# Optimization experiments

Hardware: AMD Instinct MI355X
Metric: run time of the kernel (lower is better)

Reference implementation:

```python
import jax, jax.numpy as jnp
import numpy as np

D_MODEL = 1024
D_INNER = 2048      # expand=2
D_STATE = 128
NHEADS = 32
HEADDIM = 64
DCONV = 4
CONV_DIM = D_INNER + 2 * D_STATE                 # x, B, C channels through conv
D_IN_PROJ = 2 * D_INNER + 2 * D_STATE + NHEADS   # z, xBC, dt
NBLOCKS = 4


def _mlp(x, w1, b1, w2, b2):
    # MLP(2, in, out): Linear(in,in) -> ReLU -> Linear(in,out)
    return jax.nn.relu(x @ w1 + b1) @ w2 + b2


def _mamba2_block(u, Wi, cw, cb, dtb, Alog, Dsk, nw, Wo):
    B, L, _ = u.shape
    zxbcdt = u @ Wi                                        # [B,L,D_IN_PROJ]
    z, xBC, dt = jnp.split(zxbcdt, [D_INNER, D_INNER + CONV_DIM], axis=-1)
    # causal depthwise conv1d, kernel 4
    pad = jnp.pad(xBC, ((0, 0), (DCONV - 1, 0), (0, 0)))
    conv = cb
    for k in range(DCONV):
        conv = conv + pad[:, k:k + L, :] * cw[:, k]
    xBC = jax.nn.silu(conv)
    xh, Bm, Cm = jnp.split(xBC, [D_INNER, D_INNER + D_STATE], axis=-1)
    dt = jax.nn.softplus(dt + dtb)                         # [B,L,H]
    A = -jnp.exp(Alog)                                     # [H], negative
    xh = xh.reshape(B, L, NHEADS, HEADDIM)

    def step(h, inp):
        x_t, dt_t, b_t, c_t = inp                          # [B,H,P],[B,H],[B,N],[B,N]
        dA = jnp.exp(dt_t * A)                             # [B,H]
        h = h * dA[..., None, None] + (dt_t[..., None] * x_t)[..., None] * b_t[:, None, None, :]
        y = jnp.einsum('bhpn,bn->bhp', h, c_t)
        return h, y

    h0 = jnp.zeros((B, NHEADS, HEADDIM, D_STATE), u.dtype)
    _, ys = jax.lax.scan(step, h0, (xh.transpose(1, 0, 2, 3), dt.transpose(1, 0, 2),
                                    Bm.transpose(1, 0, 2), Cm.transpose(1, 0, 2)))
    y = ys.transpose(1, 0, 2, 3) + Dsk[None, None, :, None] * xh   # D skip per head
    y = y.reshape(B, L, D_INNER)
    y = y * jax.nn.silu(z)                                 # gated RMSNorm (gate before norm)
    y = y * jax.lax.rsqrt(jnp.mean(y * y, axis=-1, keepdims=True) + 1e-5) * nw
    return y @ Wo


def setup_inputs() -> dict:
    key = jax.random.key(0)
    ks = jax.random.split(key, 16)
    B, S, STATE = 4, 512, 510
    s = 0.02
    return {
        'x': jax.random.normal(ks[0], (B, S, STATE), jnp.float32),
        'steps_left': jax.random.uniform(ks[1], (B, S, 1), jnp.float32) * 100.0,
        'current_r': jax.random.normal(ks[2], (B, S, 1), jnp.float32),
        'mlp_in_w1': jax.random.normal(ks[3], (STATE + 2, STATE + 2), jnp.float32) * s,
        'mlp_in_b1': jnp.zeros((STATE + 2,), jnp.float32),
        'mlp_in_w2': jax.random.normal(ks[4], (STATE + 2, D_MODEL), jnp.float32) * s,
        'mlp_in_b2': jnp.zeros((D_MODEL,), jnp.float32),
        'W_in': jax.random.normal(ks[5], (NBLOCKS, D_MODEL, D_IN_PROJ), jnp.float32) * s,
        'conv_w': jax.random.normal(ks[6], (NBLOCKS, CONV_DIM, DCONV), jnp.float32) * 0.2,
        'conv_b': jnp.zeros((NBLOCKS, CONV_DIM), jnp.float32),
        'dt_bias': jax.random.normal(ks[7], (NBLOCKS, NHEADS), jnp.float32) * 0.1,
        'A_log': jnp.log(jax.random.uniform(ks[8], (NBLOCKS, NHEADS), jnp.float32, 1.0, 16.0)),
        'D_skip': jnp.ones((NBLOCKS, NHEADS), jnp.float32),
        'norm_w': jnp.ones((NBLOCKS, D_INNER), jnp.float32),
        'W_out': jax.random.normal(ks[9], (NBLOCKS, D_INNER, D_MODEL), jnp.float32) * s,
        'mlp_out_w1': jax.random.normal(ks[10], (D_MODEL, D_MODEL), jnp.float32) * s,
        'mlp_out_b1': jnp.zeros((D_MODEL,), jnp.float32),
        'mlp_out_w2': jax.random.normal(ks[11], (D_MODEL, 1), jnp.float32) * s,
        'mlp_out_b2': jnp.zeros((1,), jnp.float32),
    }


def reference(x, steps_left, current_r,
              mlp_in_w1, mlp_in_b1, mlp_in_w2, mlp_in_b2,
              W_in, conv_w, conv_b, dt_bias, A_log, D_skip, norm_w, W_out,
              mlp_out_w1, mlp_out_b1, mlp_out_w2, mlp_out_b2):
    h = jnp.concatenate([x, steps_left, current_r], axis=-1)   # [B,S,state+2]
    h = _mlp(h, mlp_in_w1, mlp_in_b1, mlp_in_w2, mlp_in_b2)
    for i in range(NBLOCKS):
        h = _mamba2_block(h, W_in[i], conv_w[i], conv_b[i], dt_bias[i],
                          A_log[i], D_skip[i], norm_w[i], W_out[i])
    return _mlp(h, mlp_out_w1, mlp_out_b1, mlp_out_w2, mlp_out_b2)  # [B,S,1]
```

## Files before the change

### kernel.cpp

```cpp
#include <hip/hip_runtime.h>
#include <hip/hip_bf16.h>
#include <math.h>

#define D_MODEL   1024
#define D_INNER   2048
#define D_STATE   128
#define NHEADS    32
#define HEADDIM   64
#define DCONV     4
#define CONV_DIM  (D_INNER + 2 * D_STATE)
#define D_IN_PROJ (2 * D_INNER + 2 * D_STATE + NHEADS)
#define NBLOCKS   4
#define BATCH     4
#define SEQ       512
#define NTOK      (BATCH * SEQ)
#define STATE_IN  510
#define NPAD_IN   4480
#define NSEG      8
#define SEGLEN    64
#define NBH       (BATCH * NHEADS)
#define OFF_B     D_INNER
#define OFF_C     (D_INNER + D_STATE)
#define OFF_DT    (D_IN_PROJ - NHEADS)

typedef _Float16 half8_t __attribute__((ext_vector_type(8)));
typedef float f32x4_t  __attribute__((ext_vector_type(4)));
typedef unsigned short us;
typedef unsigned short us8 __attribute__((ext_vector_type(8)));

__device__ __forceinline__ us f2h(float f) {
    _Float16 h = (_Float16)f;
    return __builtin_bit_cast(us, h);
}
__device__ __forceinline__ float h2f(us u) {
    return (float)__builtin_bit_cast(_Float16, u);
}
__device__ __forceinline__ void gl2lds16(const us* gp, us* lp) {
    __builtin_amdgcn_global_load_lds(
        (const __attribute__((address_space(1))) unsigned int*)(gp),
        (__attribute__((address_space(3))) unsigned int*)(lp), 16, 0, 0);
}

__global__ void concat_kernel(const float* __restrict__ x,
                              const float* __restrict__ steps,
                              const float* __restrict__ curr,
                              us* __restrict__ hcat)
{
    int idx = blockIdx.x * 256 + threadIdx.x;
    if (idx >= NTOK * 512) return;
    int bl = idx >> 9;
    int c  = idx & 511;
    float v;
    if (c < STATE_IN)       v = x[(size_t)bl * STATE_IN + c];
    else if (c == STATE_IN) v = steps[bl];
    else                    v = curr[bl];
    hcat[idx] = f2h(v);
}

#define NT_TRANS 6976
__global__ __launch_bounds__(256)
void transpose_all_kernel(const float* __restrict__ mi_w1, const float* __restrict__ mi_w2,
                          const float* __restrict__ W_in, const float* __restrict__ W_out,
                          const float* __restrict__ mo_w1,
                          us* __restrict__ wt_mi1, us* __restrict__ wt_mi2,
                          us* __restrict__ wt_in, us* __restrict__ wt_out,
                          us* __restrict__ wt_mo1)
{
    int bid = blockIdx.x;
    const float* W; us* WT; int K, N, ntx, r;
    if (bid < 64)        { W = mi_w1; WT = wt_mi1; K = 512;  N = 512;  ntx = 8;  r = bid; }
    else if (bid < 192)  { W = mi_w2; WT = wt_mi2; K = 512;  N = 1024; ntx = 16; r = bid - 64; }
    else if (bid < 4672) {
        int rel = bid - 192, i = rel / 1120;
        r = rel - i * 1120;
        W  = W_in  + (size_t)i * D_MODEL * D_IN_PROJ;
        WT = wt_in + (size_t)i * NPAD_IN * 1024;
        K = 1024; N = D_IN_PROJ; ntx = 70;
    }
    else if (bid < 6720) {
        int rel = bid - 4672, i = rel / 512;
        r = rel - i * 512;
        W  = W_out  + (size_t)i * D_INNER * D_MODEL;
        WT = wt_out + (size_t)i * 1024 * 2048;
        K = 2048; N = 1024; ntx = 16;
    }
    else { W = mo_w1; WT = wt_mo1; K = 1024; N = 1024; ntx = 16; r = bid - 6720; }
    int n0 = (r % ntx) * 64, k0 = (r / ntx) * 64;

    __shared__ float tile[64][65];
    int t = threadIdx.x;
    int kl = t >> 4;
    int nl = (t & 15) * 4;
#pragma unroll
    for (int it = 0; it < 4; ++it) {
        int k = kl + it * 16;
        float4 v = make_float4(0.f, 0.f, 0.f, 0.f);
        if (n0 + nl < N) v = *(const float4*)(W + (size_t)(k0 + k) * N + n0 + nl);
        tile[k][nl + 0] = v.x; tile[k][nl + 1] = v.y;
        tile[k][nl + 2] = v.z; tile[k][nl + 3] = v.w;
    }
    __syncthreads();
    int a  = t & 7;
    int nr = t >> 3;
#pragma unroll
    for (int s = 0; s < 2; ++s) {
        int n = nr + s * 32;
        us8 o;
#pragma unroll
        for (int j = 0; j < 8; ++j) o[j] = f2h(tile[a * 8 + j][n]);
        *(us8*)(WT + (size_t)(n0 + n) * K + k0 + a * 8) = o;
    }
}

#define PHASE(TT, CUR, STG)                                                     \
    {                                                                           \
        if ((TT) == NT - 1)                                                     \
            asm volatile("s_waitcnt vmcnt(0)" ::: "memory");                    \
        else if constexpr (BM / 64 + BN / 64 == 4)                              \
            asm volatile("s_waitcnt vmcnt(4)" ::: "memory");                    \
        else if constexpr (BM / 64 + BN / 64 == 3)                              \
            asm volatile("s_waitcnt vmcnt(3)" ::: "memory");                    \
        else                                                                    \
            asm volatile("s_waitcnt vmcnt(2)" ::: "memory");                    \
        __builtin_amdgcn_s_barrier();                                           \
        if ((TT) + 2 < NT) stage(STG, ((TT) + 2) << 5);                         \
        half8_t af[TI], bfr[4];                                                 \
        _Pragma("unroll")                                                       \
        for (int ti = 0; ti < TI; ++ti) {                                       \
            int rr = wr + ti * 16 + l16;                                        \
            af[ti] = *(const half8_t*)&Al[CUR][rr * 32 + ((g ^ ((rr >> 2) & 3)) * 8)]; \
        }                                                                       \
        _Pragma("unroll")                                                       \
        for (int tj = 0; tj < 4; ++tj) {                                        \
            int rr = wc + tj * 16 + l16;                                        \
            bfr[tj] = *(const half8_t*)&Bl[CUR][rr * 32 + ((g ^ ((rr >> 2) & 3)) * 8)]; \
        }                                                                       \
        _Pragma("unroll")                                                       \
        for (int ti = 0; ti < TI; ++ti)                                         \
            _Pragma("unroll")                                                   \
            for (int tj = 0; tj < 4; ++tj)                                      \
                acc[ti][tj] = __builtin_amdgcn_mfma_f32_16x16x32_f16(           \
                    af[ti], bfr[tj], acc[ti][tj], 0, 0, 0);                     \
    }

template<int BM, int BN, int TI>
__global__ __launch_bounds__(256)
void mfma_gemm_f16(const us* __restrict__ A, const us* __restrict__ BT,
                   const float* __restrict__ bias, us* __restrict__ C,
                   int N, int K, int relu)
{
    __shared__ __attribute__((aligned(16))) us Al[3][BM * 32];
    __shared__ __attribute__((aligned(16))) us Bl[3][BN * 32];
    const int tid = threadIdx.x, lane = tid & 63, wave = tid >> 6;
    const int g = lane >> 4, l16 = lane & 15;
    const int wr = (BN == 128) ? (wave >> 1) * 64 : wave * (BM / 4);
    const int wc = (BN == 128) ? (wave & 1) * 64 : 0;
    const int m0 = blockIdx.y * BM, n0 = blockIdx.x * BN;
    const int lrow = lane >> 2;
    const int lcol = ((lane & 3) ^ ((lrow >> 2) & 3)) * 8;

    f32x4_t acc[TI][4];
    const f32x4_t zero = {0.f, 0.f, 0.f, 0.f};
#pragma unroll
    for (int i = 0; i < TI; ++i)
#pragma unroll
        for (int j = 0; j < 4; ++j) acc[i][j] = zero;

    const us* abase = A  + (size_t)m0 * K;
    const us* bbase = BT + (size_t)n0 * K;

    auto stage = [&](int buf, int k0) {
#pragma unroll
        for (int s = 0; s < BM / 64; ++s) {
            int rb = wave * (BM / 4) + s * 16;
            gl2lds16(abase + (size_t)(rb + lrow) * K + k0 + lcol, &Al[buf][rb * 32]);
        }
#pragma unroll
        for (int s = 0; s < BN / 64; ++s) {
            int rb = wave * (BN / 4) + s * 16;
            gl2lds16(bbase + (size_t)(rb + lrow) * K + k0 + lcol, &Bl[buf][rb * 32]);
        }
    };

    const int NT = K >> 5;
    stage(0, 0);
    stage(1, 32);

    for (int t = 0; t < NT; t += 3) {
        PHASE(t, 0, 2)
        if (t + 1 < NT) PHASE(t + 1, 1, 0)
        if (t + 2 < NT) PHASE(t + 2, 2, 1)
    }

#pragma unroll
    for (int tj = 0; tj < 4; ++tj) {
        int col = n0 + wc + tj * 16 + l16;
        if (col >= N) continue;
        float bv = bias ? bias[col] : 0.f;
#pragma unroll
        for (int ti = 0; ti < TI; ++ti) {
            int rbase = m0 + wr + ti * 16 + g * 4;
#pragma unroll
            for (int r = 0; r < 4; ++r) {
                float v = acc[ti][tj][r] + bv;
                if (relu) v = fmaxf(v, 0.f);
                C[(size_t)(rbase + r) * N + col] = f2h(v);
            }
        }
    }
}

__global__ __launch_bounds__(256)
void conv_silu_kernel(const us* __restrict__ zxbcdt,
                      const float* __restrict__ cw,
                      const float* __restrict__ cb,
                      us* __restrict__ xBCc)
{
    int idx = blockIdx.x * 256 + threadIdx.x;
    if (idx >= NTOK * (CONV_DIM / 4)) return;
    int cq = idx % (CONV_DIM / 4);
    int bl = idx / (CONV_DIM / 4);
    int b  = bl >> 9;
    int l  = bl & 511;
    int c  = cq * 4;
    float4 w0 = *(const float4*)&cw[(c + 0) * DCONV];
    float4 w1 = *(const float4*)&cw[(c + 1) * DCONV];
    float4 w2 = *(const float4*)&cw[(c + 2) * DCONV];
    float4 w3 = *(const float4*)&cw[(c + 3) * DCONV];
    float4 bb = *(const float4*)&cb[c];
    float a0 = bb.x, a1 = bb.y, a2 = bb.z, a3 = bb.w;
    const us* base = zxbcdt + (size_t)(b * SEQ) * D_IN_PROJ + D_INNER + c;
#pragma unroll
    for (int k = 0; k < DCONV; ++k) {
        int ll = l + k - (DCONV - 1);
        if (ll >= 0) {
            ushort4 u = *(const ushort4*)(base + (size_t)ll * D_IN_PROJ);
            a0 = fmaf(h2f(u.x), ((const float*)&w0)[k], a0);
            a1 = fmaf(h2f(u.y), ((const float*)&w1)[k], a1);
            a2 = fmaf(h2f(u.z), ((const float*)&w2)[k], a2);
            a3 = fmaf(h2f(u.w), ((const float*)&w3)[k], a3);
        }
    }
    ushort4 o;
    o.x = f2h(a0 / (1.f + __expf(-a0)));
    o.y = f2h(a1 / (1.f + __expf(-a1)));
    o.z = f2h(a2 / (1.f + __expf(-a2)));
    o.w = f2h(a3 / (1.f + __expf(-a3)));
    *(ushort4*)(xBCc + (size_t)bl * CONV_DIM + c) = o;
}

__global__ __launch_bounds__(256)
void scan_seg_mfma_kernel(const us* __restrict__ zx, const us* __restrict__ xc,
                          const float* __restrict__ dt_bias,
                          const float* __restrict__ A_log,
                          const float* __restrict__ D_skip,
                          float* __restrict__ y, float* __restrict__ alpha,
                          us* __restrict__ Hseg)
{
    __shared__ __attribute__((aligned(16))) us Csh[64 * 128];
    __shared__ __attribute__((aligned(16))) us Bsh[64 * 128];
    __shared__ __attribute__((aligned(16))) us Bt[128 * 64];
    __shared__ __attribute__((aligned(16))) us Xt[64 * 64];
    __shared__ float dt_s[64], ls[64], csc[64];
    us* Ssh = Csh;
    const int bi = blockIdx.x, bh = bi >> 3, seg = bi & 7;
    const int b = bh >> 5, h = bh & 31;
    const int tid = threadIdx.x, lane = tid & 63, w = tid >> 6;
    const int g = lane >> 4, l16 = lane & 15;
    const int t0g = seg * SEGLEN;
    const size_t rowbase = (size_t)(b * SEQ + t0g);

    {
        int rr = lane >> 4, s = lane & 15;
#pragma unroll
        for (int it = 0; it < 4; ++it) {
            int rb = w * 16 + it * 4;
            int row = rb + rr;
            const us* src = xc + (rowbase + row) * CONV_DIM;
            int sw = (s ^ (row & 7)) * 8;
            gl2lds16(src + OFF_C + sw, &Csh[rb * 128]);
            gl2lds16(src + OFF_B + sw, &Bsh[rb * 128]);
        }
    }
#pragma unroll
    for (int qi = 0; qi < 4; ++qi) {
        int idx = tid + qi * 256;
        int pq = idx & 15, j = idx >> 4;
        ushort4 v = *(const ushort4*)(xc + (rowbase + j) * CONV_DIM + h * 64 + pq * 4);
#pragma unroll
        for (int e = 0; e < 4; ++e) {
            int p = pq * 4 + e;
            int pc = ((((j >> 3) ^ (p & 7)) << 3) | (j & 7));
            Xt[p * 64 + pc] = ((const us*)&v)[e];
        }
    }
#pragma unroll
    for (int qi = 0; qi < 8; ++qi) {
        int idx = tid + qi * 256;
        int nq = idx & 31, j = idx >> 5;
        ushort4 v = *(const ushort4*)(xc + (rowbase + j) * CONV_DIM + OFF_B + nq * 4);
#pragma unroll
        for (int e = 0; e < 4; ++e) {
            int n = nq * 4 + e;
            int pc = ((((j >> 3) ^ (n & 7)) << 3) | (j & 7));
            Bt[n * 64 + pc] = ((const us*)&v)[e];
        }
    }
    if (tid < 64) {
        int j = tid;
        float dtraw = h2f(zx[(rowbase + j) * D_IN_PROJ + OFF_DT + h]) + dt_bias[h];
        float dtv = (dtraw > 20.f) ? dtraw : log1pf(expf(dtraw));
        float ld = dtv * (-expf(A_log[h]));
#pragma unroll
        for (int o = 1; o < 64; o <<= 1) {
            float v = __shfl_up(ld, o);
            if (j >= o) ld += v;
        }
        float al = expf(ld);
        dt_s[j] = dtv;
        ls[j] = ld;
        alpha[(size_t)bh * SEQ + t0g + j] = al;
        float cend = __shfl(ld, 63);
        csc[j] = dtv * expf(cend - ld);
    }
    __syncthreads();

    const float Dsk = D_skip[h];
    const f32x4_t vzero = {0.f, 0.f, 0.f, 0.f};

    f32x4_t acc1[4];
#pragma unroll
    for (int jt = 0; jt < 4; ++jt) acc1[jt] = vzero;
    {
        int ia = w * 16 + l16;
#pragma unroll
        for (int ks = 0; ks < 4; ++ks) {
            half8_t a = *(const half8_t*)&Csh[ia * 128 + (((ks * 4 + g) ^ (ia & 7)) << 3)];
#pragma unroll
            for (int jt = 0; jt < 4; ++jt) {
                int jr = jt * 16 + l16;
                half8_t bfr = *(const half8_t*)&Bsh[jr * 128 + (((ks * 4 + g) ^ (jr & 7)) << 3)];
                acc1[jt] = __builtin_amdgcn_mfma_f32_16x16x32_f16(a, bfr, acc1[jt], 0, 0, 0);
            }
        }
    }
    __syncthreads();

    {
        int i0 = w * 16 + g * 4;
        float lsi[4];
#pragma unroll
        for (int r = 0; r < 4; ++r) lsi[r] = ls[i0 + r];
#pragma unroll
        for (int jt = 0; jt < 4; ++jt) {
            int j = jt * 16 + l16;
            float lj = ls[j], dj = dt_s[j];
#pragma unroll
            for (int r = 0; r < 4; ++r) {
                int i = i0 + r;
                float v = 0.f;
                if (j < i)       v = acc1[jt][r] * dj * __expf(lsi[r] - lj);
                else if (j == i) v = acc1[jt][r] * dj + Dsk;
                int pc = ((((j >> 3) ^ (i & 7)) << 3) | (j & 7));
                Ssh[i * 64 + pc] = f2h(v);
            }
        }
    }
    __syncthreads();

    f32x4_t acc2[4];
#pragma unroll
    for (int nt = 0; nt < 4; ++nt) acc2[nt] = vzero;
    {
        int ia = w * 16 + l16;
#pragma unroll
        for (int ks = 0; ks < 2; ++ks) {
            half8_t a = *(const half8_t*)&Ssh[ia * 64 + (((ks * 4 + g) ^ (ia & 7)) << 3)];
#pragma unroll
            for (int nt = 0; nt < 4; ++nt) {
                int pr = nt * 16 + l16;
                half8_t bfr = *(const half8_t*)&Xt[pr * 64 + (((ks * 4 + g) ^ (pr & 7)) << 3)];
                acc2[nt] = __builtin_amdgcn_mfma_f32_16x16x32_f16(a, bfr, acc2[nt], 0, 0, 0);
            }
        }
    }
    {
        int i0 = w * 16 + g * 4;
#pragma unroll
        for (int nt = 0; nt < 4; ++nt) {
            int p = nt * 16 + l16;
#pragma unroll
            for (int r = 0; r < 4; ++r)
                y[(rowbase + i0 + r) * D_INNER + h * 64 + p] = acc2[nt][r];
        }
    }
    f32x4_t acc3[8];
#pragma unroll
    for (int nt = 0; nt < 8; ++nt) acc3[nt] = vzero;
    {
        int pa = w * 16 + l16;
#pragma unroll
        for (int ks = 0; ks < 2; ++ks) {
            half8_t araw = *(const half8_t*)&Xt[pa * 64 + (((ks * 4 + g) ^ (pa & 7)) << 3)];
            half8_t a;
#pragma unroll
            for (int e = 0; e < 8; ++e)
                a[e] = (_Float16)((float)araw[e] * csc[ks * 32 + g * 8 + e]);
#pragma unroll
            for (int nt = 0; nt < 8; ++nt) {
                int nr = nt * 16 + l16;
                half8_t bfr = *(const half8_t*)&Bt[nr * 64 + (((ks * 4 + g) ^ (nr & 7)) << 3)];
                acc3[nt] = __builtin_amdgcn_mfma_f32_16x16x32_f16(a, bfr, acc3[nt], 0, 0, 0);
            }
        }
    }
    {
        int p0 = w * 16 + g * 4;
#pragma unroll
        for (int nt = 0; nt < 8; ++nt) {
            int n = nt * 16 + l16;
#pragma unroll
            for (int r = 0; r < 4; ++r)
                Hseg[((size_t)bi * 64 + p0 + r) * 128 + n] = f2h(acc3[nt][r]);
        }
    }
}

__global__ __launch_bounds__(512)
void state_fixup_kernel(const float* __restrict__ alpha, us* __restrict__ Hseg)
{
    const int bh = blockIdx.x >> 1, hf = blockIdx.x & 1;
    const int t = threadIdx.x, p = t >> 3, ng = t & 7;
    const int off = hf * 64 + ng * 8;
    float carry[8];
#pragma unroll
    for (int j = 0; j < 8; ++j) carry[j] = 0.f;
    for (int seg = 0; seg < NSEG; ++seg) {
        us* hs = Hseg + (((size_t)bh * NSEG + seg) * 64 + p) * 128 + off;
        float ae = alpha[(size_t)bh * SEQ + seg * SEGLEN + SEGLEN - 1];
        float tmp[8];
#pragma unroll
        for (int q = 0; q < 2; ++q) {
            ushort4 u = *(const ushort4*)(hs + q * 4);
            tmp[q*4+0] = h2f(u.x); tmp[q*4+1] = h2f(u.y);
            tmp[q*4+2] = h2f(u.z); tmp[q*4+3] = h2f(u.w);
        }
#pragma unroll
        for (int q = 0; q < 2; ++q) {
            ushort4 o;
            o.x = f2h(carry[q*4+0]); o.y = f2h(carry[q*4+1]);
            o.z = f2h(carry[q*4+2]); o.w = f2h(carry[q*4+3]);
            *(ushort4*)(hs + q * 4) = o;
        }
#pragma unroll
        for (int j = 0; j < 8; ++j) carry[j] = fmaf(carry[j], ae, tmp[j]);
    }
}

__global__ __launch_bounds__(256)
void correct_mfma_kernel(const us* __restrict__ xc, const float* __restrict__ alpha,
                         const us* __restrict__ Hseg, float* __restrict__ y)
{
    __shared__ __attribute__((aligned(16))) us Csh[64 * 128];
    __shared__ __attribute__((aligned(16))) us Hsh[64 * 128];
    __shared__ float als_s[64];
    const int bi = blockIdx.x;
    const int bh = bi / 7, seg = 1 + (bi % 7);
    const int b = bh >> 5, h = bh & 31;
    const int tid = threadIdx.x, lane = tid & 63, w = tid >> 6;
    const int g = lane >> 4, l16 = lane & 15;
    const int t0g = seg * SEGLEN;
    const size_t rowbase = (size_t)(b * SEQ + t0g);
    const size_t hbase = (size_t)(bh * NSEG + seg) * 64;

    {
        int rr = lane >> 4, s = lane & 15;
#pragma unroll
        for (int it = 0; it < 4; ++it) {
            int rb = w * 16 + it * 4;
            int row = rb + rr;
            int sw = (s ^ (row & 7)) * 8;
            gl2lds16(xc + (rowbase + row) * CONV_DIM + OFF_C + sw, &Csh[rb * 128]);
            gl2lds16(Hseg + (hbase + row) * 128 + sw, &Hsh[rb * 128]);
        }
    }
    if (tid < 64) als_s[tid] = alpha[(size_t)bh * SEQ + t0g + tid];
    __syncthreads();

    const f32x4_t vzero = {0.f, 0.f, 0.f, 0.f};
    f32x4_t acc[4];
#pragma unroll
    for (int nt = 0; nt < 4; ++nt) acc[nt] = vzero;
    int ia = w * 16 + l16;
#pragma unroll
    for (int ks = 0; ks < 4; ++ks) {
        half8_t a = *(const half8_t*)&Csh[ia * 128 + (((ks * 4 + g) ^ (ia & 7)) << 3)];
#pragma unroll
        for (int nt = 0; nt < 4; ++nt) {
            int pr = nt * 16 + l16;
            half8_t bfr = *(const half8_t*)&Hsh[pr * 128 + (((ks * 4 + g) ^ (pr & 7)) << 3)];
            acc[nt] = __builtin_amdgcn_mfma_f32_16x16x32_f16(a, bfr, acc[nt], 0, 0, 0);
        }
    }
    int i0 = w * 16 + g * 4;
#pragma unroll
    for (int nt = 0; nt < 4; ++nt) {
        int p = nt * 16 + l16;
#pragma unroll
        for (int r = 0; r < 4; ++r) {
            size_t idx = (rowbase + i0 + r) * D_INNER + h * 64 + p;
            y[idx] += als_s[i0 + r] * acc[nt][r];
        }
    }
}

__global__ __launch_bounds__(256)
void gated_rmsnorm_kernel(const float* __restrict__ y,
                          const us* __restrict__ zxbcdt,
                          const float* __restrict__ norm_w,
                          us* __restrict__ yn)
{
    int bl = blockIdx.x;
    int t  = threadIdx.x;
    const float* yr = y + (size_t)bl * D_INNER;
    const us* zr = zxbcdt + (size_t)bl * D_IN_PROJ;
    us* outr = yn + (size_t)bl * D_INNER;

    float gv[8];
    float ss = 0.f;
#pragma unroll
    for (int q = 0; q < 8; ++q) {
        int j = t + q * 256;
        float z = h2f(zr[j]);
        float g = yr[j] * (z / (1.f + __expf(-z)));
        gv[q] = g;
        ss += g * g;
    }
    __shared__ float red[256];
    red[t] = ss;
    __syncthreads();
    for (int w = 128; w > 0; w >>= 1) {
        if (t < w) red[t] += red[t + w];
        __syncthreads();
    }
    float rs = rsqrtf(red[0] / (float)D_INNER + 1e-5f);
#pragma unroll
    for (int q = 0; q < 8; ++q) {
        int j = t + q * 256;
        outr[j] = f2h(gv[q] * rs * norm_w[j]);
    }
}

__global__ __launch_bounds__(256)
void final_dot_kernel(const us* __restrict__ t1,
                      const float* __restrict__ w2,
                      const float* __restrict__ b2,
                      float* __restrict__ out)
{
    int bl = blockIdx.x;
    int t  = threadIdx.x;
    float s = 0.f;
    for (int j = t; j < D_MODEL; j += 256)
        s = fmaf(h2f(t1[(size_t)bl * D_MODEL + j]), w2[j], s);
    __shared__ float red[256];
    red[t] = s;
    __syncthreads();
    for (int w = 128; w > 0; w >>= 1) {
        if (t < w) red[t] += red[t + w];
        __syncthreads();
    }
    if (t == 0) out[bl] = red[0] + b2[0];
}

extern "C" void kernel_launch(void* const* d_in, const int* in_sizes, int n_in,
                              void* d_out, int out_size, void* d_ws, size_t ws_size,
                              hipStream_t stream)
{
    const float* x        = (const float*)d_in[0];
    const float* steps    = (const float*)d_in[1];
    const float* curr     = (const float*)d_in[2];
    const float* mi_w1    = (const float*)d_in[3];
    const float* mi_b1    = (const float*)d_in[4];
    const float* mi_w2    = (const float*)d_in[5];
    const float* mi_b2    = (const float*)d_in[6];
    const float* W_in     = (const float*)d_in[7];
    const float* conv_w   = (const float*)d_in[8];
    const float* conv_b   = (const float*)d_in[9];
    const float* dt_bias  = (const float*)d_in[10];
    const float* A_log    = (const float*)d_in[11];
    const float* D_skip   = (const float*)d_in[12];
    const float* norm_w   = (const float*)d_in[13];
    const float* W_out    = (const float*)d_in[14];
    const float* mo_w1    = (const float*)d_in[15];
    const float* mo_b1    = (const float*)d_in[16];
    const float* mo_w2    = (const float*)d_in[17];
    const float* mo_b2    = (const float*)d_in[18];
    float* out = (float*)d_out;

    us* wt_mi1 = (us*)d_ws;
    us* wt_mi2 = wt_mi1 + (size_t)512 * 512;
    us* wt_in  = wt_mi2 + (size_t)1024 * 512;
    us* wt_out = wt_in  + (size_t)4 * NPAD_IN * 1024;
    us* wt_mo1 = wt_out + (size_t)4 * 1024 * 2048;
    us* Hseg   = wt_mo1 + (size_t)1024 * 1024;
    us* hcat   = Hseg   + (size_t)NBH * NSEG * 64 * 128;
    us* h      = hcat   + (size_t)NTOK * 512;
    us* zxb    = h      + (size_t)NTOK * D_MODEL;
    us* xc     = zxb    + (size_t)NTOK * D_IN_PROJ;
    us* yn     = xc     + (size_t)NTOK * CONV_DIM;
    us* t0     = zxb;
    us* t1     = xc;
    float* fbase = (float*)((((uintptr_t)(yn + (size_t)NTOK * D_INNER)) + 255)
                            & ~(uintptr_t)255);
    float* y     = fbase;
    float* alpha = y + (size_t)NTOK * D_INNER;

    transpose_all_kernel<<<NT_TRANS, 256, 0, stream>>>(
        mi_w1, mi_w2, W_in, W_out, mo_w1,
        wt_mi1, wt_mi2, wt_in, wt_out, wt_mo1);

    concat_kernel<<<(NTOK * 512 + 255) / 256, 256, 0, stream>>>(x, steps, curr, hcat);

    mfma_gemm_f16<64, 64, 1><<<dim3(512/64, NTOK/64), 256, 0, stream>>>(
        hcat, wt_mi1, mi_b1, t0, 512, 512, 1);
    mfma_gemm_f16<64, 64, 1><<<dim3(1024/64, NTOK/64), 256, 0, stream>>>(
        t0, wt_mi2, mi_b2, h, 1024, 512, 0);

    for (int i = 0; i < NBLOCKS; ++i) {
        mfma_gemm_f16<128, 128, 4><<<dim3(NPAD_IN/128, NTOK/128), 256, 0, stream>>>(
            h, wt_in + (size_t)i * NPAD_IN * 1024, nullptr, zxb, D_IN_PROJ, D_MODEL, 0);
        conv_silu_kernel<<<(NTOK * (CONV_DIM/4) + 255) / 256, 256, 0, stream>>>(
            zxb, conv_w + (size_t)i * CONV_DIM * DCONV, conv_b + (size_t)i * CONV_DIM, xc);
        scan_seg_mfma_kernel<<<NBH * NSEG, 256, 0, stream>>>(
            zxb, xc, dt_bias + i * NHEADS, A_log + i * NHEADS, D_skip + i * NHEADS,
            y, alpha, Hseg);
        state_fixup_kernel<<<NBH * 2, 512, 0, stream>>>(alpha, Hseg);
        correct_mfma_kernel<<<NBH * (NSEG - 1), 256, 0, stream>>>(xc, alpha, Hseg, y);
        gated_rmsnorm_kernel<<<NTOK, 256, 0, stream>>>(
            y, zxb, norm_w + (size_t)i * D_INNER, yn);
        mfma_gemm_f16<128, 64, 2><<<dim3(1024/64, NTOK/128), 256, 0, stream>>>(
            yn, wt_out + (size_t)i * 1024 * 2048, nullptr, h, 1024, 2048, 0);
    }

    mfma_gemm_f16<128, 64, 2><<<dim3(1024/64, NTOK/128), 256, 0, stream>>>(
        h, wt_mo1, mo_b1, t1, 1024, 1024, 1);
    final_dot_kernel<<<NTOK, 256, 0, stream>>>(t1, mo_w2, mo_b2, out);
}
```

Before: 734.2 us.

## Rewrite weight transpose as register-only 128x64 tiles, shrink out-proj GEMM tiles

The weight transpose kernel drops its shared-memory tile. Each thread now loads eight float4 rows into registers and writes four 8-wide f16 columns directly, which halves the block count and removes the barrier. Separately, the W_out projection and output MLP GEMMs switch from 128x64 to 64x64 tiles, doubling the grid to improve occupancy on the many-CU device. The register transpose gives up coalescing on both reads and writes, since each warp reads strided rows, and smaller tiles reduce data reuse.

```diff
diff --git a/kernel.cpp b/kernel.cpp
--- a/kernel.cpp
+++ b/kernel.cpp
@@ -57,7 +57,7 @@
     hcat[idx] = f2h(v);
 }
 
-#define NT_TRANS 6976
+#define NT_TRANS 3488
 __global__ __launch_bounds__(256)
 void transpose_all_kernel(const float* __restrict__ mi_w1, const float* __restrict__ mi_w2,
                           const float* __restrict__ W_in, const float* __restrict__ W_out,
@@ -68,47 +68,47 @@
 {
     int bid = blockIdx.x;
     const float* W; us* WT; int K, N, ntx, r;
-    if (bid < 64)        { W = mi_w1; WT = wt_mi1; K = 512;  N = 512;  ntx = 8;  r = bid; }
-    else if (bid < 192)  { W = mi_w2; WT = wt_mi2; K = 512;  N = 1024; ntx = 16; r = bid - 64; }
-    else if (bid < 4672) {
-        int rel = bid - 192, i = rel / 1120;
-        r = rel - i * 1120;
+    if (bid < 32)        { W = mi_w1; WT = wt_mi1; K = 512;  N = 512;  ntx = 4; r = bid; }
+    else if (bid < 96)   { W = mi_w2; WT = wt_mi2; K = 512;  N = 1024; ntx = 8; r = bid - 32; }
+    else if (bid < 2336) {
+        int rel = bid - 96, i = rel / 560;
+        r = rel - i * 560;
         W  = W_in  + (size_t)i * D_MODEL * D_IN_PROJ;
         WT = wt_in + (size_t)i * NPAD_IN * 1024;
-        K = 1024; N = D_IN_PROJ; ntx = 70;
-    }
-    else if (bid < 6720) {
-        int rel = bid - 4672, i = rel / 512;
-        r = rel - i * 512;
+        K = 1024; N = D_IN_PROJ; ntx = 35;
+    }
+    else if (bid < 3360) {
+        int rel = bid - 2336, i = rel / 256;
+        r = rel - i * 256;
         W  = W_out  + (size_t)i * D_INNER * D_MODEL;
         WT = wt_out + (size_t)i * 1024 * 2048;
-        K = 2048; N = 1024; ntx = 16;
-    }
-    else { W = mo_w1; WT = wt_mo1; K = 1024; N = 1024; ntx = 16; r = bid - 6720; }
-    int n0 = (r % ntx) * 64, k0 = (r / ntx) * 64;
-
-    __shared__ float tile[64][65];
+        K = 2048; N = 1024; ntx = 8;
+    }
+    else { W = mo_w1; WT = wt_mo1; K = 1024; N = 1024; ntx = 8; r = bid - 3360; }
+    int n0 = (r % ntx) * 128, k0 = (r / ntx) * 64;
+
     int t = threadIdx.x;
-    int kl = t >> 4;
-    int nl = (t & 15) * 4;
-#pragma unroll
-    for (int it = 0; it < 4; ++it) {
-        int k = kl + it * 16;
-        float4 v = make_float4(0.f, 0.f, 0.f, 0.f);
-        if (n0 + nl < N) v = *(const float4*)(W + (size_t)(k0 + k) * N + n0 + nl);
-        tile[k][nl + 0] = v.x; tile[k][nl + 1] = v.y;
-        tile[k][nl + 2] = v.z; tile[k][nl + 3] = v.w;
-    }
-    __syncthreads();
-    int a  = t & 7;
-    int nr = t >> 3;
-#pragma unroll
-    for (int s = 0; s < 2; ++s) {
-        int n = nr + s * 32;
+    int ko = t & 7;
+    int nq = t >> 3;
+    int n  = n0 + nq * 4;
+    int k  = k0 + ko * 8;
+
+    float4 v[8];
+    if (n < N) {
+        const float* src = W + (size_t)k * N + n;
+#pragma unroll
+        for (int j = 0; j < 8; ++j)
+            v[j] = *(const float4*)(src + (size_t)j * N);
+    } else {
+#pragma unroll
+        for (int j = 0; j < 8; ++j) v[j] = make_float4(0.f, 0.f, 0.f, 0.f);
+    }
+#pragma unroll
+    for (int q = 0; q < 4; ++q) {
         us8 o;
 #pragma unroll
-        for (int j = 0; j < 8; ++j) o[j] = f2h(tile[a * 8 + j][n]);
-        *(us8*)(WT + (size_t)(n0 + n) * K + k0 + a * 8) = o;
+        for (int j = 0; j < 8; ++j) o[j] = f2h(((const float*)&v[j])[q]);
+        *(us8*)(WT + (size_t)(n + q) * K + k) = o;
     }
 }
 
@@ -638,11 +638,11 @@
         correct_mfma_kernel<<<NBH * (NSEG - 1), 256, 0, stream>>>(xc, alpha, Hseg, y);
         gated_rmsnorm_kernel<<<NTOK, 256, 0, stream>>>(
             y, zxb, norm_w + (size_t)i * D_INNER, yn);
-        mfma_gemm_f16<128, 64, 2><<<dim3(1024/64, NTOK/128), 256, 0, stream>>>(
+        mfma_gemm_f16<64, 64, 1><<<dim3(1024/64, NTOK/64), 256, 0, stream>>>(
             yn, wt_out + (size_t)i * 1024 * 2048, nullptr, h, 1024, 2048, 0);
     }
 
-    mfma_gemm_f16<128, 64, 2><<<dim3(1024/64, NTOK/128), 256, 0, stream>>>(
+    mfma_gemm_f16<64, 64, 1><<<dim3(1024/64, NTOK/64), 256, 0, stream>>>(
         h, wt_mo1, mo_b1, t1, 1024, 1024, 1);
     final_dot_kernel<<<NTOK, 256, 0, stream>>>(t1, mo_w2, mo_b2, out);
 }
```

Measured after the change: 722.8 us. Within noise of the previous version (-1.6%).
